# Optimization experiments

Measured on AMD Instinct MI355X. Metric: run time of the kernel, lower is better.

## Reference

```python
import jax, jax.numpy as jnp
import numpy as np

KSIZE = 3
RES_SCALE = 0.2
WITH_RESIDUAL = True


def setup_inputs() -> dict:
    key = jax.random.key(0)
    x = jax.random.normal(key, (8, 3, 1024, 1024), dtype=jnp.float32)
    return {"x": x}


def reference(x) -> jnp.ndarray:
    B, C, H, W = x.shape
    k = KSIZE
    p = k // 2
    # zero padding matches F.unfold(padding=k//2)
    xp = jnp.pad(x, ((0, 0), (0, 0), (p, p), (p, p)))
    # [B, C, k*k, H, W] stack of shifted views (k*k = 9, small static loop)
    patches = jnp.stack(
        [xp[:, :, di:di + H, dj:dj + W] for di in range(k) for dj in range(k)],
        axis=2,
    )
    # median of odd-sized window = middle element of sorted values
    med = jnp.sort(patches, axis=2)[:, :, (k * k) // 2]
    if WITH_RESIDUAL:
        return x + RES_SCALE * (med - x)
    return med
```

## Files before the change

### kernel.cpp

```cpp
#include <hip/hip_runtime.h>


typedef float v4f __attribute__((ext_vector_type(4)));

#define S2(a,b) { float _t=fminf(a,b); (b)=fmaxf(a,b); (a)=_t; }
__device__ __forceinline__ float med3f(float a, float b, float c) {
    return fmaxf(fminf(a, b), fminf(fmaxf(a, b), c));
}

constexpr int W = 1024, H = 1024;

__global__ __launch_bounds__(256, 8) void median_blur_kernel(
    const float* __restrict__ xin, float* __restrict__ out)
{
    const unsigned orig  = blockIdx.x;
    const unsigned chunk = gridDim.x >> 3;
    const unsigned wg    = (orig & 7u) * chunk + (orig >> 3);
    const int y = (int)(wg & (unsigned)(H - 1));
    const size_t plane = (size_t)(wg >> 10) * (size_t)(H * W);

    const int tx   = threadIdx.x;
    const int lane = tx & 63;
    const int x0   = tx << 2;
    const float* base = xin + plane;

    const int yt = y > 0     ? y - 1 : 0;
    const int yb = y < H - 1 ? y + 1 : H - 1;
    const float* rpt = base + ((size_t)yt << 10);
    const float* rpm = base + ((size_t)y  << 10);
    const float* rpb = base + ((size_t)yb << 10);

    v4f ct = *reinterpret_cast<const v4f*>(rpt + x0);
    v4f cm = *reinterpret_cast<const v4f*>(rpm + x0);
    v4f cb = *reinterpret_cast<const v4f*>(rpb + x0);

    float hlt = __shfl_up(ct.w, 1);
    float hlm = __shfl_up(cm.w, 1);
    float hlb = __shfl_up(cb.w, 1);
    float hrt = __shfl_down(ct.x, 1);
    float hrm = __shfl_down(cm.x, 1);
    float hrb = __shfl_down(cb.x, 1);
    if (lane == 0) {
        if (tx == 0) { hlt = 0.0f; hlm = 0.0f; hlb = 0.0f; }
        else         { hlt = rpt[x0 - 1]; hlm = rpm[x0 - 1]; hlb = rpb[x0 - 1]; }
    }
    if (lane == 63) {
        if (tx == 255) { hrt = 0.0f; hrm = 0.0f; hrb = 0.0f; }
        else           { hrt = rpt[x0 + 4]; hrm = rpm[x0 + 4]; hrb = rpb[x0 + 4]; }
    }

    float t[6] = { hlt, ct.x, ct.y, ct.z, ct.w, hrt };
    float m[6] = { hlm, cm.x, cm.y, cm.z, cm.w, hrm };
    float b[6] = { hlb, cb.x, cb.y, cb.z, cb.w, hrb };
    if (y == 0) {
#pragma unroll
        for (int j = 0; j < 6; ++j) t[j] = 0.0f;
    }
    if (y == H - 1) {
#pragma unroll
        for (int j = 0; j < 6; ++j) b[j] = 0.0f;
    }

    float lo[6], mi[6], hi[6];
#pragma unroll
    for (int j = 0; j < 6; ++j) {
        float a = t[j], c0 = m[j], d = b[j];
        S2(a, c0); S2(c0, d); S2(a, c0);
        lo[j] = a; mi[j] = c0; hi[j] = d;
    }
    v4f o;
#pragma unroll
    for (int j = 0; j < 4; ++j) {
        const float mxlo = fmaxf(lo[j], fmaxf(lo[j + 1], lo[j + 2]));
        const float mnhi = fminf(hi[j], fminf(hi[j + 1], hi[j + 2]));
        const float mdmi = med3f(mi[j], mi[j + 1], mi[j + 2]);
        const float med  = med3f(mxlo, mdmi, mnhi);
        const float xc   = m[j + 1];
        o[j] = xc + 0.2f * (med - xc);
    }
    *reinterpret_cast<v4f*>(out + plane + ((size_t)y << 10) + x0) = o;
}

extern "C" void kernel_launch(void* const* d_in, const int* in_sizes, int n_in,
                              void* d_out, int out_size, void* d_ws, size_t ws_size,
                              hipStream_t stream) {
    const float* x = (const float*)d_in[0];
    float* out = (float*)d_out;
    const int planes = in_sizes[0] / (H * W);
    dim3 block(256);
    dim3 grid(planes * H);
    median_blur_kernel<<<grid, block, 0, stream>>>(x, out);
}
```

Baseline: 179.1 us.

## Compute four output rows per block to reuse vertically overlapping input rows

Each workgroup now produces four consecutive output rows and loads six input rows once, instead of loading three rows for each single output row. This cuts redundant global/L2 reads of overlapping rows from 3x to 1.5x and reduces the block count fourfold. In exchange it raises register use, and the launch-bounds occupancy hint is lowered to match.

```diff
diff --git a/kernel.cpp b/kernel.cpp
--- a/kernel.cpp
+++ b/kernel.cpp
@@ -9,76 +9,75 @@
 }
 
 constexpr int W = 1024, H = 1024;
+constexpr int RPB = 4;
+constexpr int NR  = RPB + 2;
 
-__global__ __launch_bounds__(256, 8) void median_blur_kernel(
+__global__ __launch_bounds__(256, 6) void median_blur_kernel(
     const float* __restrict__ xin, float* __restrict__ out)
 {
     const unsigned orig  = blockIdx.x;
     const unsigned chunk = gridDim.x >> 3;
     const unsigned wg    = (orig & 7u) * chunk + (orig >> 3);
-    const int y = (int)(wg & (unsigned)(H - 1));
-    const size_t plane = (size_t)(wg >> 10) * (size_t)(H * W);
+    const int    y0    = (int)((wg & 255u) << 2);
+    const size_t plane = (size_t)(wg >> 8) * (size_t)(H * W);
 
     const int tx   = threadIdx.x;
     const int lane = tx & 63;
     const int x0   = tx << 2;
     const float* base = xin + plane;
 
-    const int yt = y > 0     ? y - 1 : 0;
-    const int yb = y < H - 1 ? y + 1 : H - 1;
-    const float* rpt = base + ((size_t)yt << 10);
-    const float* rpm = base + ((size_t)y  << 10);
-    const float* rpb = base + ((size_t)yb << 10);
-
-    v4f ct = *reinterpret_cast<const v4f*>(rpt + x0);
-    v4f cm = *reinterpret_cast<const v4f*>(rpm + x0);
-    v4f cb = *reinterpret_cast<const v4f*>(rpb + x0);
-
-    float hlt = __shfl_up(ct.w, 1);
-    float hlm = __shfl_up(cm.w, 1);
-    float hlb = __shfl_up(cb.w, 1);
-    float hrt = __shfl_down(ct.x, 1);
-    float hrm = __shfl_down(cm.x, 1);
-    float hrb = __shfl_down(cb.x, 1);
-    if (lane == 0) {
-        if (tx == 0) { hlt = 0.0f; hlm = 0.0f; hlb = 0.0f; }
-        else         { hlt = rpt[x0 - 1]; hlm = rpm[x0 - 1]; hlb = rpb[x0 - 1]; }
-    }
-    if (lane == 63) {
-        if (tx == 255) { hrt = 0.0f; hrm = 0.0f; hrb = 0.0f; }
-        else           { hrt = rpt[x0 + 4]; hrm = rpm[x0 + 4]; hrb = rpb[x0 + 4]; }
+    v4f c[NR];
+#pragma unroll
+    for (int s = 0; s < NR; ++s) {
+        int y = y0 - 1 + s;
+        y = y < 0 ? 0 : (y > H - 1 ? H - 1 : y);
+        c[s] = *reinterpret_cast<const v4f*>(base + ((size_t)y << 10) + x0);
     }
 
-    float t[6] = { hlt, ct.x, ct.y, ct.z, ct.w, hrt };
-    float m[6] = { hlm, cm.x, cm.y, cm.z, cm.w, hrm };
-    float b[6] = { hlb, cb.x, cb.y, cb.z, cb.w, hrb };
-    if (y == 0) {
+    float hl[NR], hr[NR];
 #pragma unroll
-        for (int j = 0; j < 6; ++j) t[j] = 0.0f;
-    }
-    if (y == H - 1) {
-#pragma unroll
-        for (int j = 0; j < 6; ++j) b[j] = 0.0f;
+    for (int s = 0; s < NR; ++s) {
+        int y = y0 - 1 + s;
+        y = y < 0 ? 0 : (y > H - 1 ? H - 1 : y);
+        const float* rp = base + ((size_t)y << 10);
+        hl[s] = __shfl_up(c[s].w, 1);
+        hr[s] = __shfl_down(c[s].x, 1);
+        if (lane == 0)  hl[s] = (tx == 0)   ? 0.0f : rp[x0 - 1];
+        if (lane == 63) hr[s] = (tx == 255) ? 0.0f : rp[x0 + 4];
     }
 
-    float lo[6], mi[6], hi[6];
+    if (y0 == 0) {
+        c[0] = (v4f){0.0f, 0.0f, 0.0f, 0.0f}; hl[0] = 0.0f; hr[0] = 0.0f;
+    }
+    if (y0 == H - RPB) {
+        c[NR-1] = (v4f){0.0f, 0.0f, 0.0f, 0.0f}; hl[NR-1] = 0.0f; hr[NR-1] = 0.0f;
+    }
+
 #pragma unroll
-    for (int j = 0; j < 6; ++j) {
-        float a = t[j], c0 = m[j], d = b[j];
-        S2(a, c0); S2(c0, d); S2(a, c0);
-        lo[j] = a; mi[j] = c0; hi[j] = d;
+    for (int r = 0; r < RPB; ++r) {
+        const float t[6] = { hl[r],   c[r].x,   c[r].y,   c[r].z,   c[r].w,   hr[r]   };
+        const float m[6] = { hl[r+1], c[r+1].x, c[r+1].y, c[r+1].z, c[r+1].w, hr[r+1] };
+        const float b[6] = { hl[r+2], c[r+2].x, c[r+2].y, c[r+2].z, c[r+2].w, hr[r+2] };
+
+        float lo[6], mi[6], hi[6];
+#pragma unroll
+        for (int j = 0; j < 6; ++j) {
+            float a = t[j], c0 = m[j], d = b[j];
+            S2(a, c0); S2(c0, d); S2(a, c0);
+            lo[j] = a; mi[j] = c0; hi[j] = d;
+        }
+        v4f o;
+#pragma unroll
+        for (int j = 0; j < 4; ++j) {
+            const float mxlo = fmaxf(lo[j], fmaxf(lo[j + 1], lo[j + 2]));
+            const float mnhi = fminf(hi[j], fminf(hi[j + 1], hi[j + 2]));
+            const float mdmi = med3f(mi[j], mi[j + 1], mi[j + 2]);
+            const float med  = med3f(mxlo, mdmi, mnhi);
+            const float xc   = m[j + 1];
+            o[j] = xc + 0.2f * (med - xc);
+        }
+        *reinterpret_cast<v4f*>(out + plane + ((size_t)(y0 + r) << 10) + x0) = o;
     }
-    v4f o;
-#pragma unroll
-    for (int j = 0; j < 4; ++j) {
-        const float mxlo = fmaxf(lo[j], fmaxf(lo[j + 1], lo[j + 2]));
-        const float mnhi = fminf(hi[j], fminf(hi[j + 1], hi[j + 2]));
-        const float mdmi = med3f(mi[j], mi[j + 1], mi[j + 2]);
-        const float med  = med3f(mxlo, mdmi, mnhi);
-        const float xc   = m[j + 1];
-        o[j] = xc + 0.2f * (med - xc);
-    }
-    *reinterpret_cast<v4f*>(out + plane + ((size_t)y << 10) + x0) = o;
 }
 
 extern "C" void kernel_launch(void* const* d_in, const int* in_sizes, int n_in,
@@ -88,6 +87,6 @@
     float* out = (float*)d_out;
     const int planes = in_sizes[0] / (H * W);
     dim3 block(256);
-    dim3 grid(planes * H);
+    dim3 grid(planes * (H / RPB));
     median_blur_kernel<<<grid, block, 0, stream>>>(x, out);
 }
```

Measured after the change: 176.7 us. About the same (-1.4%).

## Assign one full row per wavefront to remove cross-wave halo loads

Applied to the files above, without the earlier changes.

Each wavefront now handles a whole 1024-wide row in four 256-column segments, instead of each block handling one row split across four waves. Halo values between segments come from wave-wide shuffles of lane 0 and lane 63, so the scalar global halo loads at wave boundaries go away. The grid shrinks by a factor of four and launch bounds drop to 6 waves per EU to allow more registers. The trade-offs are higher register pressure, twelve vector loads in flight per thread, and a different blockIdx-to-XCD swizzle granularity.

```diff
diff --git a/kernel.cpp b/kernel.cpp
--- a/kernel.cpp
+++ b/kernel.cpp
@@ -10,19 +10,21 @@
 
 constexpr int W = 1024, H = 1024;
 
-__global__ __launch_bounds__(256, 8) void median_blur_kernel(
+__global__ __launch_bounds__(256, 6) void median_blur_kernel(
     const float* __restrict__ xin, float* __restrict__ out)
 {
     const unsigned orig  = blockIdx.x;
     const unsigned chunk = gridDim.x >> 3;
     const unsigned wg    = (orig & 7u) * chunk + (orig >> 3);
-    const int y = (int)(wg & (unsigned)(H - 1));
-    const size_t plane = (size_t)(wg >> 10) * (size_t)(H * W);
 
     const int tx   = threadIdx.x;
+    const int wv   = tx >> 6;
     const int lane = tx & 63;
-    const int x0   = tx << 2;
-    const float* base = xin + plane;
+
+    const unsigned g = wg * 4u + (unsigned)wv;
+    const int    y     = (int)(g & 1023u);
+    const size_t plane = (size_t)(g >> 10) * (size_t)(H * W);
+    const float* base  = xin + plane;
 
     const int yt = y > 0     ? y - 1 : 0;
     const int yb = y < H - 1 ? y + 1 : H - 1;
@@ -30,55 +32,67 @@
     const float* rpm = base + ((size_t)y  << 10);
     const float* rpb = base + ((size_t)yb << 10);
 
-    v4f ct = *reinterpret_cast<const v4f*>(rpt + x0);
-    v4f cm = *reinterpret_cast<const v4f*>(rpm + x0);
-    v4f cb = *reinterpret_cast<const v4f*>(rpb + x0);
+    const int xo = lane << 2;
 
-    float hlt = __shfl_up(ct.w, 1);
-    float hlm = __shfl_up(cm.w, 1);
-    float hlb = __shfl_up(cb.w, 1);
-    float hrt = __shfl_down(ct.x, 1);
-    float hrm = __shfl_down(cm.x, 1);
-    float hrb = __shfl_down(cb.x, 1);
-    if (lane == 0) {
-        if (tx == 0) { hlt = 0.0f; hlm = 0.0f; hlb = 0.0f; }
-        else         { hlt = rpt[x0 - 1]; hlm = rpm[x0 - 1]; hlb = rpb[x0 - 1]; }
-    }
-    if (lane == 63) {
-        if (tx == 255) { hrt = 0.0f; hrm = 0.0f; hrb = 0.0f; }
-        else           { hrt = rpt[x0 + 4]; hrm = rpm[x0 + 4]; hrb = rpb[x0 + 4]; }
+    v4f ct[4], cm[4], cb[4];
+#pragma unroll
+    for (int j = 0; j < 4; ++j) {
+        ct[j] = *reinterpret_cast<const v4f*>(rpt + (j << 8) + xo);
+        cm[j] = *reinterpret_cast<const v4f*>(rpm + (j << 8) + xo);
+        cb[j] = *reinterpret_cast<const v4f*>(rpb + (j << 8) + xo);
     }
 
-    float t[6] = { hlt, ct.x, ct.y, ct.z, ct.w, hrt };
-    float m[6] = { hlm, cm.x, cm.y, cm.z, cm.w, hrm };
-    float b[6] = { hlb, cb.x, cb.y, cb.z, cb.w, hrb };
     if (y == 0) {
 #pragma unroll
-        for (int j = 0; j < 6; ++j) t[j] = 0.0f;
+        for (int j = 0; j < 4; ++j) ct[j] = (v4f){0.0f, 0.0f, 0.0f, 0.0f};
     }
     if (y == H - 1) {
 #pragma unroll
-        for (int j = 0; j < 6; ++j) b[j] = 0.0f;
+        for (int j = 0; j < 4; ++j) cb[j] = (v4f){0.0f, 0.0f, 0.0f, 0.0f};
     }
 
-    float lo[6], mi[6], hi[6];
-#pragma unroll
-    for (int j = 0; j < 6; ++j) {
-        float a = t[j], c0 = m[j], d = b[j];
-        S2(a, c0); S2(c0, d); S2(a, c0);
-        lo[j] = a; mi[j] = c0; hi[j] = d;
-    }
-    v4f o;
+    float* o_row = out + plane + ((size_t)y << 10);
+
 #pragma unroll
     for (int j = 0; j < 4; ++j) {
-        const float mxlo = fmaxf(lo[j], fmaxf(lo[j + 1], lo[j + 2]));
-        const float mnhi = fminf(hi[j], fminf(hi[j + 1], hi[j + 2]));
-        const float mdmi = med3f(mi[j], mi[j + 1], mi[j + 2]);
-        const float med  = med3f(mxlo, mdmi, mnhi);
-        const float xc   = m[j + 1];
-        o[j] = xc + 0.2f * (med - xc);
+        float tl_u = __shfl_up(ct[j].w, 1), ml_u = __shfl_up(cm[j].w, 1), bl_u = __shfl_up(cb[j].w, 1);
+        float tl_b = (j > 0) ? __shfl(ct[j - 1].w, 63) : 0.0f;
+        float ml_b = (j > 0) ? __shfl(cm[j - 1].w, 63) : 0.0f;
+        float bl_b = (j > 0) ? __shfl(cb[j - 1].w, 63) : 0.0f;
+        const float tl = (lane == 0) ? tl_b : tl_u;
+        const float ml = (lane == 0) ? ml_b : ml_u;
+        const float bl = (lane == 0) ? bl_b : bl_u;
+        float tr_d = __shfl_down(ct[j].x, 1), mr_d = __shfl_down(cm[j].x, 1), br_d = __shfl_down(cb[j].x, 1);
+        float tr_b = (j < 3) ? __shfl(ct[j + 1].x, 0) : 0.0f;
+        float mr_b = (j < 3) ? __shfl(cm[j + 1].x, 0) : 0.0f;
+        float br_b = (j < 3) ? __shfl(cb[j + 1].x, 0) : 0.0f;
+        const float tr = (lane == 63) ? tr_b : tr_d;
+        const float mr = (lane == 63) ? mr_b : mr_d;
+        const float br = (lane == 63) ? br_b : br_d;
+
+        const float t[6] = { tl, ct[j].x, ct[j].y, ct[j].z, ct[j].w, tr };
+        const float m[6] = { ml, cm[j].x, cm[j].y, cm[j].z, cm[j].w, mr };
+        const float b[6] = { bl, cb[j].x, cb[j].y, cb[j].z, cb[j].w, br };
+
+        float lo[6], mi[6], hi[6];
+#pragma unroll
+        for (int q = 0; q < 6; ++q) {
+            float a = t[q], c0 = m[q], d = b[q];
+            S2(a, c0); S2(c0, d); S2(a, c0);
+            lo[q] = a; mi[q] = c0; hi[q] = d;
+        }
+        v4f o;
+#pragma unroll
+        for (int q = 0; q < 4; ++q) {
+            const float mxlo = fmaxf(lo[q], fmaxf(lo[q + 1], lo[q + 2]));
+            const float mnhi = fminf(hi[q], fminf(hi[q + 1], hi[q + 2]));
+            const float mdmi = med3f(mi[q], mi[q + 1], mi[q + 2]);
+            const float med  = med3f(mxlo, mdmi, mnhi);
+            const float xc   = m[q + 1];
+            o[q] = xc + 0.2f * (med - xc);
+        }
+        *reinterpret_cast<v4f*>(o_row + (j << 8) + xo) = o;
     }
-    *reinterpret_cast<v4f*>(out + plane + ((size_t)y << 10) + x0) = o;
 }
 
 extern "C" void kernel_launch(void* const* d_in, const int* in_sizes, int n_in,
@@ -88,6 +102,6 @@
     float* out = (float*)d_out;
     const int planes = in_sizes[0] / (H * W);
     dim3 block(256);
-    dim3 grid(planes * H);
+    dim3 grid(planes * (H / 4));
     median_blur_kernel<<<grid, block, 0, stream>>>(x, out);
 }
```

After: 174.3 us. 1.03x faster.
